# Kernel tuning notes

Hardware: AMD Instinct MI355X
Metric: run time of the kernel (lower is better)

Reference implementation:

```python
import jax, jax.numpy as jnp
import numpy as np

B, S, D, H, L, NITEMS = 512, 200, 64, 2, 2, 100000
HD = D // H
EPS = 1e-8
C = 0.001


def _ln(x, w, b):
    m = jnp.mean(x, -1, keepdims=True)
    v = jnp.mean((x - m) ** 2, -1, keepdims=True)
    return (x - m) / jnp.sqrt(v + EPS) * w + b


def _frob(x):
    return jnp.sqrt(jnp.sum(x * x))


def setup_inputs() -> dict:
    key = jax.random.key(0)
    ks = jax.random.split(key, 20)
    rn = lambda k, shape, s=0.02: jax.random.normal(k, shape, jnp.float32) * s
    item_emb = rn(ks[0], (NITEMS + 1, D))
    pos_emb = rn(ks[1], (S + 1, D)).at[0].set(0.0)  # padding_idx=0 row
    pred_w = rn(ks[2], (1, D))
    inp = {
        'user_ids': jax.random.randint(ks[3], (B,), 0, NITEMS, dtype=jnp.int32),
        'log_seqs': jax.random.randint(ks[4], (B, S), 0, NITEMS + 1, dtype=jnp.int32),
        'pos_seqs': jax.random.randint(ks[5], (B, S), 0, NITEMS + 1, dtype=jnp.int32),
        'item_emb': item_emb, 'pos_emb': pos_emb, 'pred_w': pred_w,
        'ln_w': jnp.ones((L, D), jnp.float32), 'ln_b': rn(ks[6], (L, D)),
        'qkv_w': rn(ks[7], (L, 3 * D, D)), 'qkv_b': rn(ks[8], (L, 3 * D)),
        'out_w': rn(ks[9], (L, D, D)), 'out_b': rn(ks[10], (L, D)),
        'fc1_w': rn(ks[11], (L, D, D)), 'fc1_b': rn(ks[12], (L, D)),
        'ffln_w': jnp.ones((L, D), jnp.float32), 'ffln_b': rn(ks[13], (L, D)),
        'fc2_w': rn(ks[14], (L, D, D)), 'fc2_b': rn(ks[15], (L, D)),
        'ffln2_w': jnp.ones((L, D), jnp.float32), 'ffln2_b': rn(ks[16], (L, D)),
    }
    return inp


def reference(user_ids, log_seqs, pos_seqs, item_emb, pos_emb, pred_w,
              ln_w, ln_b, qkv_w, qkv_b, out_w, out_b,
              fc1_w, fc1_b, ffln_w, ffln_b, fc2_w, fc2_b, ffln2_w, ffln2_b):
    # ---- log2feats ----
    x = item_emb[log_seqs] * jnp.sqrt(jnp.float32(D))  # (B,S,D)
    poss = jnp.arange(1, S + 1, dtype=log_seqs.dtype)[None, :] * (log_seqs != 0)
    x = x + pos_emb[poss]
    causal_bias = jnp.where(jnp.tril(jnp.ones((S, S), bool)), 0.0, -1e30).astype(jnp.float32)
    for l in range(L):
        q_in = _ln(x, ln_w[l], ln_b[l])  # query uses pre-LN, K/V use raw seqs
        q = (q_in @ qkv_w[l, :D].T + qkv_b[l, :D]).reshape(B, S, H, HD)
        k = (x @ qkv_w[l, D:2 * D].T + qkv_b[l, D:2 * D]).reshape(B, S, H, HD)
        v = (x @ qkv_w[l, 2 * D:].T + qkv_b[l, 2 * D:]).reshape(B, S, H, HD)
        sc = jnp.einsum('bqhd,bkhd->bhqk', q, k) / jnp.sqrt(jnp.float32(HD)) + causal_bias
        a = jax.nn.softmax(sc, -1)
        ctx = jnp.einsum('bhqk,bkhd->bqhd', a, v).reshape(B, S, D)
        x = q_in + ctx @ out_w[l].T + out_b[l]
        h = jax.nn.relu(_ln(x, ffln_w[l], ffln_b[l]) @ fc1_w[l].T + fc1_b[l])
        x = h @ fc2_w[l].T + fc2_b[l] + _ln(x, ffln2_w[l], ffln2_b[l])
    # ---- left(): quadratic form via Gram matrices (math identical to outer-product sum) ----
    FF = jnp.einsum('bsi,bsj->ij', x, x)          # sum_b F_b^T F_b  (d,d)
    EE = item_emb.T @ item_emb                      # (d,d)
    hh = pred_w.T @ pred_w                          # (d,d)
    left = C * jnp.sum(FF * EE * hh)
    # ---- right() ----
    ps = (x * item_emb[pos_seqs]) @ pred_w[0]       # (B,S), prediction has no bias
    right = jnp.sum((1.0 - C) * ps ** 2 - 2.0 * ps)
    # ---- reg_loss(): sum of per-parameter Frobenius norms ----
    reg = _frob(item_emb) + _frob(pos_emb) + _frob(pred_w)
    for p in (ln_w, ln_b, qkv_w, qkv_b, out_w, out_b, fc1_w, fc1_b,
              ffln_w, ffln_b, fc2_w, fc2_b, ffln2_w, ffln2_b):
        reg = reg + jnp.sum(jax.vmap(_frob)(p))  # per-layer params are separate tensors
    return left + right + 0.1 * reg
```

## Files before the change

kernel.cpp:

```cpp
#include <hip/hip_runtime.h>
#include <math.h>

#define BB 512
#define SS 200
#define DDIM 64
#define HD 32
#define LL 2
#define NROWS (BB * SS)
#define EPS 1e-8f
#define CC 0.001f
#define GRAM_NB 256
#define LSTRIDE 72
#define XS 68

typedef __attribute__((ext_vector_type(8))) short bf16x8;
typedef __attribute__((ext_vector_type(4))) float f32x4;

__device__ unsigned short g_qb[NROWS * DDIM];
__device__ float g_gpart[2 * GRAM_NB * 4096];
__device__ unsigned short g_wb[49152];

__device__ __forceinline__ float wave_sum(float v) {
#pragma unroll
    for (int o = 32; o > 0; o >>= 1) v += __shfl_xor(v, o, 64);
    return v;
}
__device__ __forceinline__ unsigned short f2b(float f) {
    unsigned u = __float_as_uint(f);
    return (unsigned short)((u + 0x7FFFu + ((u >> 16) & 1u)) >> 16);
}

__global__ __launch_bounds__(256) void prep_weights(const float* __restrict__ qkv_w,
                                                    const float* __restrict__ out_w,
                                                    const float* __restrict__ fc1_w,
                                                    const float* __restrict__ fc2_w,
                                                    unsigned short* __restrict__ wb) {
    int i4 = (blockIdx.x * 256 + threadIdx.x) * 4;
    const float* src; int off;
    if (i4 < 24576)      { src = qkv_w; off = 0; }
    else if (i4 < 32768) { src = out_w; off = 24576; }
    else if (i4 < 40960) { src = fc1_w; off = 32768; }
    else                 { src = fc2_w; off = 40960; }
    float4 f = *(const float4*)&src[i4 - off];
    ushort4 o; o.x = f2b(f.x); o.y = f2b(f.y); o.z = f2b(f.z); o.w = f2b(f.w);
    *(ushort4*)&wb[i4] = o;
}

__device__ __forceinline__ bf16x8 frag_raw(const float* Xf, int row, int c0) {
    const float* p = &Xf[row * XS + c0];
    float4 u = *(const float4*)p;
    float4 v = *(const float4*)(p + 4);
    bf16x8 r;
    r[0] = (short)f2b(u.x); r[1] = (short)f2b(u.y); r[2] = (short)f2b(u.z); r[3] = (short)f2b(u.w);
    r[4] = (short)f2b(v.x); r[5] = (short)f2b(v.y); r[6] = (short)f2b(v.z); r[7] = (short)f2b(v.w);
    return r;
}
__device__ __forceinline__ bf16x8 frag_ln(const float* Xf, const float* stats,
                                          const float* vw, const float* vb,
                                          int row, int c0) {
    float m = stats[row * 2], rs = stats[row * 2 + 1];
    const float* p = &Xf[row * XS + c0];
    float4 u = *(const float4*)p;
    float4 v = *(const float4*)(p + 4);
    bf16x8 r;
    r[0] = (short)f2b((u.x - m) * rs * vw[c0 + 0] + vb[c0 + 0]);
    r[1] = (short)f2b((u.y - m) * rs * vw[c0 + 1] + vb[c0 + 1]);
    r[2] = (short)f2b((u.z - m) * rs * vw[c0 + 2] + vb[c0 + 2]);
    r[3] = (short)f2b((u.w - m) * rs * vw[c0 + 3] + vb[c0 + 3]);
    r[4] = (short)f2b((v.x - m) * rs * vw[c0 + 4] + vb[c0 + 4]);
    r[5] = (short)f2b((v.y - m) * rs * vw[c0 + 5] + vb[c0 + 5]);
    r[6] = (short)f2b((v.z - m) * rs * vw[c0 + 6] + vb[c0 + 6]);
    r[7] = (short)f2b((v.w - m) * rs * vw[c0 + 7] + vb[c0 + 7]);
    return r;
}

__device__ __forceinline__ void gemm_acc(bf16x8 a0, bf16x8 a1, const unsigned short* W,
                                         int m16, int quad, f32x4 acc[4]) {
#pragma unroll
    for (int nt = 0; nt < 4; ++nt) {
        bf16x8 b0 = *(const bf16x8*)&W[(nt * 16 + m16) * LSTRIDE + quad * 8];
        bf16x8 b1 = *(const bf16x8*)&W[(nt * 16 + m16) * LSTRIDE + 32 + quad * 8];
        acc[nt] = __builtin_amdgcn_mfma_f32_16x16x32_bf16(a0, b0, acc[nt], 0, 0, 0);
        acc[nt] = __builtin_amdgcn_mfma_f32_16x16x32_bf16(a1, b1, acc[nt], 0, 0, 0);
    }
}

__device__ __forceinline__ void stage_w512(const unsigned short* G, unsigned short* L, int t) {
#pragma unroll
    for (int rep = 0; rep < 2; ++rep) {
        int idx = t + rep * 512;
        int r = idx >> 4, c4 = (idx & 15) * 4;
        *(ushort4*)&L[r * LSTRIDE + c4] = *(const ushort4*)&G[r * 64 + c4];
    }
}

__global__ __launch_bounds__(512) void mega(const int* __restrict__ log_seqs,
                                            const int* __restrict__ pos_seqs,
                                            const float* __restrict__ item_emb,
                                            const float* __restrict__ pos_emb,
                                            const float* __restrict__ pred_w,
                                            const float* __restrict__ ln_w,  const float* __restrict__ ln_b,
                                            const float* __restrict__ qkv_b,
                                            const float* __restrict__ out_b,
                                            const float* __restrict__ fc1_b, const float* __restrict__ fc2_b,
                                            const float* __restrict__ ffln_w, const float* __restrict__ ffln_b,
                                            const float* __restrict__ ffln2_w, const float* __restrict__ ffln2_b,
                                            const unsigned short* __restrict__ wb,
                                            unsigned short* __restrict__ xb,
                                            float* __restrict__ rpart) {
    __shared__ float Xf[200 * XS];
    __shared__ unsigned short Qb[200 * 72];
    __shared__ unsigned short Kb[200 * 72];
    __shared__ unsigned short Vt[64 * 232];
    __shared__ unsigned short Wb[64 * LSTRIDE];
    __shared__ float stats[200 * 2];
    __shared__ float vecs[13][64];
    __shared__ float redw[8];

    const int t = threadIdx.x, b = blockIdx.x;
    const int w = t >> 6, lane = t & 63, m16 = lane & 15, quad = lane >> 4;
    const f32x4 Z = {0.f, 0.f, 0.f, 0.f};

    if (t < 64) vecs[12][t] = pred_w[t];

    for (int half = 0; half < 2; ++half) {
        int rr = (t >> 2) + half * 128;
        if (rr < 200) {
            int li = log_seqs[b * SS + rr];
            int poss = li ? (rr + 1) : 0;
            int qd = (t & 3) * 16;
            float4 v[4];
#pragma unroll
            for (int g = 0; g < 4; ++g) {
                float4 e = *(const float4*)&item_emb[(long)li * DDIM + qd + g * 4];
                float4 p = *(const float4*)&pos_emb[(long)poss * DDIM + qd + g * 4];
                v[g].x = e.x * 8.0f + p.x; v[g].y = e.y * 8.0f + p.y;
                v[g].z = e.z * 8.0f + p.z; v[g].w = e.w * 8.0f + p.w;
                *(float4*)&Xf[rr * XS + qd + g * 4] = v[g];
            }
            float s1 = 0.f, s2 = 0.f;
#pragma unroll
            for (int g = 0; g < 4; ++g) {
                s1 += (v[g].x + v[g].y) + (v[g].z + v[g].w);
                s2 += (v[g].x * v[g].x + v[g].y * v[g].y) + (v[g].z * v[g].z + v[g].w * v[g].w);
            }
            s1 += __shfl_xor(s1, 1, 64); s1 += __shfl_xor(s1, 2, 64);
            s2 += __shfl_xor(s2, 1, 64); s2 += __shfl_xor(s2, 2, 64);
            float mean = s1 * (1.f / 64.f);
            float var = s2 * (1.f / 64.f) - mean * mean;
            float rs = rsqrtf(var + EPS);
            if ((t & 3) == 0) { stats[rr * 2] = mean; stats[rr * 2 + 1] = rs; }
        }
    }
    __syncthreads();

    for (int l = 0; l < LL; ++l) {
        if (t < 64) {
            vecs[0][t] = qkv_b[l * 192 + t];
            vecs[1][t] = qkv_b[l * 192 + 64 + t];
            vecs[2][t] = qkv_b[l * 192 + 128 + t];
            vecs[3][t] = ln_w[l * 64 + t];   vecs[4][t] = ln_b[l * 64 + t];
            vecs[5][t] = out_b[l * 64 + t];
            vecs[6][t] = fc1_b[l * 64 + t];  vecs[7][t] = fc2_b[l * 64 + t];
            vecs[8][t] = ffln_w[l * 64 + t]; vecs[9][t] = ffln_b[l * 64 + t];
            vecs[10][t] = ffln2_w[l * 64 + t]; vecs[11][t] = ffln2_b[l * 64 + t];
        }
        stage_w512(wb + l * 12288, Wb, t);
        __syncthreads();
        for (int tb = w * 16; tb < 200; tb += 128) {
            int row = tb + m16; if (row > 199) row = 199;
            bf16x8 a0 = frag_ln(Xf, stats, vecs[3], vecs[4], row, quad * 8);
            bf16x8 a1 = frag_ln(Xf, stats, vecs[3], vecs[4], row, 32 + quad * 8);
            f32x4 acc[4] = {Z, Z, Z, Z};
            gemm_acc(a0, a1, Wb, m16, quad, acc);
#pragma unroll
            for (int nt = 0; nt < 4; ++nt) {
                int n = nt * 16 + m16; float bbv = vecs[0][n];
#pragma unroll
                for (int rg = 0; rg < 4; ++rg) {
                    int m = tb + quad * 4 + rg;
                    if (m < 200) Qb[m * 72 + n] = f2b(acc[nt][rg] + bbv);
                }
            }
        }
        __syncthreads();
        stage_w512(wb + l * 12288 + 4096, Wb, t);
        __syncthreads();
        for (int tb = w * 16; tb < 200; tb += 128) {
            int row = tb + m16; if (row > 199) row = 199;
            bf16x8 a0 = frag_raw(Xf, row, quad * 8);
            bf16x8 a1 = frag_raw(Xf, row, 32 + quad * 8);
            f32x4 acc[4] = {Z, Z, Z, Z};
            gemm_acc(a0, a1, Wb, m16, quad, acc);
#pragma unroll
            for (int nt = 0; nt < 4; ++nt) {
                int n = nt * 16 + m16; float bbv = vecs[1][n];
#pragma unroll
                for (int rg = 0; rg < 4; ++rg) {
                    int m = tb + quad * 4 + rg;
                    if (m < 200) Kb[m * 72 + n] = f2b(acc[nt][rg] + bbv);
                }
            }
        }
        __syncthreads();
        stage_w512(wb + l * 12288 + 8192, Wb, t);
        {
            int r2 = t >> 3, cc = 200 + ((t * 4) & 31);
            ushort4 z4; z4.x = z4.y = z4.z = z4.w = 0;
            *(ushort4*)&Vt[r2 * 232 + cc] = z4;
        }
        __syncthreads();
        for (int tb = w * 16; tb < 200; tb += 128) {
            int row = tb + m16; if (row > 199) row = 199;
            bf16x8 a0 = frag_raw(Xf, row, quad * 8);
            bf16x8 a1 = frag_raw(Xf, row, 32 + quad * 8);
            f32x4 acc[4] = {Z, Z, Z, Z};
            gemm_acc(a0, a1, Wb, m16, quad, acc);
#pragma unroll
            for (int nt = 0; nt < 4; ++nt) {
                int n = nt * 16 + m16; float bbv = vecs[2][n];
#pragma unroll
                for (int rg = 0; rg < 4; ++rg) {
                    int m = tb + quad * 4 + rg;
                    if (m < 200) Vt[n * 232 + m] = f2b(acc[nt][rg] + bbv);
                }
            }
        }
        __syncthreads();
        {
            unsigned short* ps = &Wb[w * 512];
            const unsigned long long s01 = 0x01030B1900020A18ull;
            const unsigned long long s23 = 0xFF050D17FF040C16ull;
            const unsigned long long s45 = 0xFF070F15FF060E14ull;
            const unsigned long long s67 = 0xFF091113FF081012ull;
            unsigned long long pair = (w & 4) ? ((w & 2) ? s67 : s45) : ((w & 2) ? s23 : s01);
            unsigned su = (unsigned)(pair >> ((w & 1) * 32));
            const float scale = 0.17677669529663687f;
            for (int slot = 0; slot < 4; ++slot) {
                int u = (su >> (slot * 8)) & 0xFF;
                if (u == 0xFF) break;
                int h = u & 1, qt = u >> 1;
                int q0 = qt * 16;
                int qrow = q0 + m16; if (qrow > 199) qrow = 199;
                bf16x8 qa = *(const bf16x8*)&Qb[qrow * 72 + h * 32 + quad * 8];
                f32x4 o0 = Z, o1 = Z;
                float lsum[4] = {0.f, 0.f, 0.f, 0.f};
                int np = (qt + 2) >> 1;
                for (int pi = 0; pi < np; ++pi) {
                    int p0 = pi * 32;
                    int kr0 = p0 + m16;      int kr0c = kr0 > 199 ? 199 : kr0;
                    int kr1 = p0 + 16 + m16; int kr1c = kr1 > 199 ? 199 : kr1;
                    bf16x8 kb0 = *(const bf16x8*)&Kb[kr0c * 72 + h * 32 + quad * 8];
                    bf16x8 kb1 = *(const bf16x8*)&Kb[kr1c * 72 + h * 32 + quad * 8];
                    f32x4 s0 = __builtin_amdgcn_mfma_f32_16x16x32_bf16(qa, kb0, Z, 0, 0, 0);
                    f32x4 s1 = __builtin_amdgcn_mfma_f32_16x16x32_bf16(qa, kb1, Z, 0, 0, 0);
                    float e0[4], e1[4];
#pragma unroll
                    for (int rg = 0; rg < 4; ++rg) {
                        int rglob = q0 + quad * 4 + rg;
                        e0[rg] = (kr0 <= rglob && kr0 < SS) ? __expf(s0[rg] * scale) : 0.f;
                        e1[rg] = (kr1 <= rglob && kr1 < SS) ? __expf(s1[rg] * scale) : 0.f;
                        lsum[rg] += e0[rg] + e1[rg];
                    }
                    __builtin_amdgcn_wave_barrier();
#pragma unroll
                    for (int rg = 0; rg < 4; ++rg) {
                        int row = quad * 4 + rg;
                        ps[row * 32 + m16] = f2b(e0[rg]);
                        ps[row * 32 + 16 + m16] = f2b(e1[rg]);
                    }
                    __builtin_amdgcn_wave_barrier();
                    bf16x8 pa = *(const bf16x8*)&ps[m16 * 32 + quad * 8];
                    bf16x8 vb0 = *(const bf16x8*)&Vt[(h * 32 + m16) * 232 + p0 + quad * 8];
                    bf16x8 vb1 = *(const bf16x8*)&Vt[(h * 32 + 16 + m16) * 232 + p0 + quad * 8];
                    o0 = __builtin_amdgcn_mfma_f32_16x16x32_bf16(pa, vb0, o0, 0, 0, 0);
                    o1 = __builtin_amdgcn_mfma_f32_16x16x32_bf16(pa, vb1, o1, 0, 0, 0);
                }
#pragma unroll
                for (int rg = 0; rg < 4; ++rg)
#pragma unroll
                    for (int o = 1; o <= 8; o <<= 1) lsum[rg] += __shfl_xor(lsum[rg], o, 64);
#pragma unroll
                for (int rg = 0; rg < 4; ++rg) {
                    int rglob = q0 + quad * 4 + rg;
                    if (rglob < SS) {
                        float inv = 1.f / lsum[rg];
                        Qb[rglob * 72 + h * 32 + m16] = f2b(o0[rg] * inv);
                        Qb[rglob * 72 + h * 32 + 16 + m16] = f2b(o1[rg] * inv);
                    }
                }
            }
        }
        __syncthreads();
        stage_w512(wb + 24576 + l * 4096, Wb, t);
        __syncthreads();
        for (int tb = w * 16; tb < 200; tb += 128) {
            int row = tb + m16; if (row > 199) row = 199;
            bf16x8 a0 = *(const bf16x8*)&Qb[row * 72 + quad * 8];
            bf16x8 a1 = *(const bf16x8*)&Qb[row * 72 + 32 + quad * 8];
            f32x4 acc[4] = {Z, Z, Z, Z};
            gemm_acc(a0, a1, Wb, m16, quad, acc);
            float x1[4][4];
#pragma unroll
            for (int nt = 0; nt < 4; ++nt) {
                int n = nt * 16 + m16;
                float bbv = vecs[5][n], lw = vecs[3][n], lb = vecs[4][n];
#pragma unroll
                for (int rg = 0; rg < 4; ++rg) {
                    int m = tb + quad * 4 + rg; int mc = m > 199 ? 199 : m;
                    float qin = (Xf[mc * XS + n] - stats[mc * 2]) * stats[mc * 2 + 1] * lw + lb;
                    x1[nt][rg] = acc[nt][rg] + bbv + qin;
                }
            }
#pragma unroll
            for (int rg = 0; rg < 4; ++rg) {
                float s1 = (x1[0][rg] + x1[1][rg]) + (x1[2][rg] + x1[3][rg]);
                float s2 = x1[0][rg] * x1[0][rg] + x1[1][rg] * x1[1][rg]
                         + x1[2][rg] * x1[2][rg] + x1[3][rg] * x1[3][rg];
#pragma unroll
                for (int o = 1; o <= 8; o <<= 1) { s1 += __shfl_xor(s1, o, 64); s2 += __shfl_xor(s2, o, 64); }
                float mean = s1 * (1.f / 64.f);
                float var = s2 * (1.f / 64.f) - mean * mean;
                float rs = rsqrtf(var + EPS);
                int m = tb + quad * 4 + rg;
                if (m < 200) {
#pragma unroll
                    for (int nt = 0; nt < 4; ++nt) Xf[m * XS + nt * 16 + m16] = x1[nt][rg];
                    if (m16 == 0) { stats[m * 2] = mean; stats[m * 2 + 1] = rs; }
                }
            }
        }
        __syncthreads();
        stage_w512(wb + 32768 + l * 4096, Wb, t);
        __syncthreads();
        for (int tb = w * 16; tb < 200; tb += 128) {
            int row = tb + m16; if (row > 199) row = 199;
            bf16x8 a0 = frag_ln(Xf, stats, vecs[8], vecs[9], row, quad * 8);
            bf16x8 a1 = frag_ln(Xf, stats, vecs[8], vecs[9], row, 32 + quad * 8);
            f32x4 acc[4] = {Z, Z, Z, Z};
            gemm_acc(a0, a1, Wb, m16, quad, acc);
#pragma unroll
            for (int nt = 0; nt < 4; ++nt) {
                int n = nt * 16 + m16; float bbv = vecs[6][n];
#pragma unroll
                for (int rg = 0; rg < 4; ++rg) {
                    int m = tb + quad * 4 + rg;
                    if (m < 200) Qb[m * 72 + n] = f2b(fmaxf(acc[nt][rg] + bbv, 0.f));
                }
            }
        }
        __syncthreads();
        stage_w512(wb + 40960 + l * 4096, Wb, t);
        __syncthreads();
        for (int tb = w * 16; tb < 200; tb += 128) {
            int row = tb + m16; if (row > 199) row = 199;
            bf16x8 a0 = *(const bf16x8*)&Qb[row * 72 + quad * 8];
            bf16x8 a1 = *(const bf16x8*)&Qb[row * 72 + 32 + quad * 8];
            f32x4 acc[4] = {Z, Z, Z, Z};
            gemm_acc(a0, a1, Wb, m16, quad, acc);
            float xn[4][4];
#pragma unroll
            for (int nt = 0; nt < 4; ++nt) {
                int n = nt * 16 + m16;
                float bbv = vecs[7][n], lw = vecs[10][n], lb = vecs[11][n];
#pragma unroll
                for (int rg = 0; rg < 4; ++rg) {
                    int m = tb + quad * 4 + rg; int mc = m > 199 ? 199 : m;
                    float ln2 = (Xf[mc * XS + n] - stats[mc * 2]) * stats[mc * 2 + 1] * lw + lb;
                    xn[nt][rg] = acc[nt][rg] + bbv + ln2;
                }
            }
#pragma unroll
            for (int rg = 0; rg < 4; ++rg) {
                float s1 = (xn[0][rg] + xn[1][rg]) + (xn[2][rg] + xn[3][rg]);
                float s2 = xn[0][rg] * xn[0][rg] + xn[1][rg] * xn[1][rg]
                         + xn[2][rg] * xn[2][rg] + xn[3][rg] * xn[3][rg];
#pragma unroll
                for (int o = 1; o <= 8; o <<= 1) { s1 += __shfl_xor(s1, o, 64); s2 += __shfl_xor(s2, o, 64); }
                float mean = s1 * (1.f / 64.f);
                float var = s2 * (1.f / 64.f) - mean * mean;
                float rs = rsqrtf(var + EPS);
                int m = tb + quad * 4 + rg;
                if (m < 200) {
#pragma unroll
                    for (int nt = 0; nt < 4; ++nt) Xf[m * XS + nt * 16 + m16] = xn[nt][rg];
                    if (m16 == 0) { stats[m * 2] = mean; stats[m * 2 + 1] = rs; }
                }
            }
        }
        __syncthreads();
    }

    for (int i = t; i < 3200; i += 512) {
        int r = i >> 4, c4 = (i & 15) * 4;
        float4 f = *(const float4*)&Xf[r * XS + c4];
        ushort4 o; o.x = f2b(f.x); o.y = f2b(f.y); o.z = f2b(f.z); o.w = f2b(f.w);
        *(ushort4*)&xb[((long)b * SS + r) * DDIM + c4] = o;
    }
    float local = 0.f;
    for (int half = 0; half < 2; ++half) {
        int rr = (t >> 2) + half * 128;
        if (rr < 200) {
            int pi = pos_seqs[b * SS + rr];
            int qd = (t & 3) * 16;
            float v = 0.f;
#pragma unroll
            for (int g = 0; g < 4; ++g) {
                float4 xv = *(const float4*)&Xf[rr * XS + qd + g * 4];
                float4 iv = *(const float4*)&item_emb[(long)pi * DDIM + qd + g * 4];
                const float* pwp = &vecs[12][qd + g * 4];
                v += xv.x * iv.x * pwp[0] + xv.y * iv.y * pwp[1]
                   + xv.z * iv.z * pwp[2] + xv.w * iv.w * pwp[3];
            }
            v += __shfl_xor(v, 1, 64); v += __shfl_xor(v, 2, 64);
            if ((t & 3) == 0) local += (1.0f - CC) * v * v - 2.0f * v;
        }
    }
    local = wave_sum(local);
    if (lane == 0) redw[w] = local;
    __syncthreads();
    if (t == 0) {
        float s = 0.f;
#pragma unroll
        for (int i = 0; i < 8; ++i) s += redw[i];
        rpart[b] = s;
    }
}

__global__ __launch_bounds__(256) void gram_kernel(const float* __restrict__ A0, int n0,
                                                   const unsigned short* __restrict__ A1, int n1,
                                                   float* __restrict__ part) {
    __shared__ unsigned short At[64 * LSTRIDE];
    int t = threadIdx.x;
    int second = blockIdx.x >= GRAM_NB;
    int bid = second ? blockIdx.x - GRAM_NB : blockIdx.x;
    int nrows = second ? n1 : n0;
    int w16 = (t >> 6) * 16, lane = t & 63, m16 = lane & 15, quad = lane >> 4;
    int bi = t & 15, bj = t >> 4;
    f32x4 zero = {0.f, 0.f, 0.f, 0.f};
    f32x4 acc[4] = {zero, zero, zero, zero};
    for (long base = (long)bid * 64; base < nrows; base += (long)GRAM_NB * 64) {
        __syncthreads();
        if (!second) {
            float rv[4][4];
#pragma unroll
            for (int e = 0; e < 4; ++e) {
                long gr = base + bj * 4 + e;
                float4 f = make_float4(0.f, 0.f, 0.f, 0.f);
                if (gr < nrows) f = *(const float4*)&A0[gr * DDIM + bi * 4];
                rv[e][0] = f.x; rv[e][1] = f.y; rv[e][2] = f.z; rv[e][3] = f.w;
            }
#pragma unroll
            for (int e = 0; e < 4; ++e) {
                ushort4 o;
                o.x = f2b(rv[0][e]); o.y = f2b(rv[1][e]); o.z = f2b(rv[2][e]); o.w = f2b(rv[3][e]);
                *(ushort4*)&At[(bi * 4 + e) * LSTRIDE + bj * 4] = o;
            }
        } else {
            ushort4 u[4];
#pragma unroll
            for (int e = 0; e < 4; ++e) {
                long gr = base + bj * 4 + e;
                ushort4 uu; uu.x = uu.y = uu.z = uu.w = 0;
                if (gr < nrows) uu = *(const ushort4*)&A1[gr * DDIM + bi * 4];
                u[e] = uu;
            }
#pragma unroll
            for (int e = 0; e < 4; ++e) {
                ushort4 o;
                o.x = ((const unsigned short*)&u[0])[e];
                o.y = ((const unsigned short*)&u[1])[e];
                o.z = ((const unsigned short*)&u[2])[e];
                o.w = ((const unsigned short*)&u[3])[e];
                *(ushort4*)&At[(bi * 4 + e) * LSTRIDE + bj * 4] = o;
            }
        }
        __syncthreads();
#pragma unroll
        for (int ks = 0; ks < 2; ++ks) {
            bf16x8 a = *(const bf16x8*)&At[(w16 + m16) * LSTRIDE + ks * 32 + quad * 8];
#pragma unroll
            for (int nt = 0; nt < 4; ++nt) {
                bf16x8 bfr = *(const bf16x8*)&At[(nt * 16 + m16) * LSTRIDE + ks * 32 + quad * 8];
                acc[nt] = __builtin_amdgcn_mfma_f32_16x16x32_bf16(a, bfr, acc[nt], 0, 0, 0);
            }
        }
    }
    float* slab = part + (long)blockIdx.x * 4096;
#pragma unroll
    for (int nt = 0; nt < 4; ++nt) {
        int n = nt * 16 + m16;
#pragma unroll
        for (int rg = 0; rg < 4; ++rg) {
            int m = w16 + quad * 4 + rg;
            slab[m * 64 + n] = acc[nt][rg];
        }
    }
}

struct NormEntry { const float* p; int n; };
struct NormArgs { NormEntry e[30]; };

__global__ __launch_bounds__(256) void reduce_norms(const float* __restrict__ part,
                                                    float* __restrict__ EE, float* __restrict__ FF,
                                                    NormArgs args, float* __restrict__ norms) {
    __shared__ float red[256];
    int blk = blockIdx.x;
    if (blk < 32) {
        int which = blk >> 4;
        int p = (blk & 15) * 256 + threadIdx.x;
        const float* basep = part + (long)which * GRAM_NB * 4096;
        float s = 0.f;
        for (int b = 0; b < GRAM_NB; ++b) s += basep[(long)b * 4096 + p];
        (which ? FF : EE)[p] = s;
    } else {
        NormEntry en = args.e[blk - 32];
        float s = 0.f;
        for (int i = threadIdx.x; i < en.n; i += 256) { float v = en.p[i]; s += v * v; }
        red[threadIdx.x] = s;
        for (int o = 128; o > 0; o >>= 1) {
            __syncthreads();
            if (threadIdx.x < o) red[threadIdx.x] += red[threadIdx.x + o];
        }
        __syncthreads();
        if (threadIdx.x == 0) norms[blk - 32] = red[0];
    }
}

__global__ __launch_bounds__(256) void final_kernel(const float* __restrict__ EE,
                                                    const float* __restrict__ FF,
                                                    const float* __restrict__ pred_w,
                                                    const float* __restrict__ rpart,
                                                    const float* __restrict__ norms,
                                                    float* __restrict__ out) {
    __shared__ float p_s[64];
    __shared__ float redL[256];
    __shared__ float redT[256];
    __shared__ float redR[256];
    int t = threadIdx.x;
    if (t < 64) p_s[t] = pred_w[t];
    __syncthreads();
    float lf = 0.f, tr = 0.f, rs = 0.f;
    for (int p = t; p < 4096; p += 256) {
        int i = p >> 6, j = p & 63;
        float ee = EE[p];
        lf += FF[p] * ee * p_s[i] * p_s[j];
        if (i == j) tr += ee;
    }
    for (int i = t; i < 512; i += 256) rs += rpart[i];
    redL[t] = lf; redT[t] = tr; redR[t] = rs;
    for (int o = 128; o > 0; o >>= 1) {
        __syncthreads();
        if (t < o) { redL[t] += redL[t + o]; redT[t] += redT[t + o]; redR[t] += redR[t + o]; }
    }
    __syncthreads();
    if (t == 0) {
        float reg = sqrtf(redT[0]);
        for (int s = 0; s < 30; ++s) reg += sqrtf(norms[s]);
        out[0] = CC * redL[0] + redR[0] + 0.1f * reg;
    }
}

struct DevPtrs { float* gpart; unsigned short *qb, *wb; };

static DevPtrs fetch_ptrs() {
    DevPtrs p;
    (void)hipGetSymbolAddress((void**)&p.gpart, HIP_SYMBOL(g_gpart));
    (void)hipGetSymbolAddress((void**)&p.qb,    HIP_SYMBOL(g_qb));
    (void)hipGetSymbolAddress((void**)&p.wb,    HIP_SYMBOL(g_wb));
    return p;
}

extern "C" void kernel_launch(void* const* d_in, const int* in_sizes, int n_in,
                              void* d_out, int out_size, void* d_ws, size_t ws_size,
                              hipStream_t stream) {
    const int*   log_seqs = (const int*)d_in[1];
    const int*   pos_seqs = (const int*)d_in[2];
    const float* item_emb = (const float*)d_in[3];
    const float* pos_emb  = (const float*)d_in[4];
    const float* pred_w   = (const float*)d_in[5];
    const float* ln_w     = (const float*)d_in[6];
    const float* ln_b     = (const float*)d_in[7];
    const float* qkv_w    = (const float*)d_in[8];
    const float* qkv_b    = (const float*)d_in[9];
    const float* out_w    = (const float*)d_in[10];
    const float* out_b    = (const float*)d_in[11];
    const float* fc1_w    = (const float*)d_in[12];
    const float* fc1_b    = (const float*)d_in[13];
    const float* ffln_w   = (const float*)d_in[14];
    const float* ffln_b   = (const float*)d_in[15];
    const float* fc2_w    = (const float*)d_in[16];
    const float* fc2_b    = (const float*)d_in[17];
    const float* ffln2_w  = (const float*)d_in[18];
    const float* ffln2_b  = (const float*)d_in[19];

    static DevPtrs P = fetch_ptrs();

    float* ws    = (float*)d_ws;
    float* rpart = ws;
    float* nrm   = ws + 1664;
    float* EE    = ws + 2048;
    float* FF    = ws + 6144;

    prep_weights<<<48, 256, 0, stream>>>(qkv_w, out_w, fc1_w, fc2_w, P.wb);

    mega<<<BB, 512, 0, stream>>>(log_seqs, pos_seqs, item_emb, pos_emb, pred_w,
                                 ln_w, ln_b, qkv_b, out_b, fc1_b, fc2_b,
                                 ffln_w, ffln_b, ffln2_w, ffln2_b,
                                 P.wb, P.qb, rpart);

    gram_kernel<<<2 * GRAM_NB, 256, 0, stream>>>(item_emb, 100001, P.qb, NROWS, P.gpart);

    NormArgs na;
    int s = 0;
    na.e[s++] = {pos_emb, (SS + 1) * DDIM};
    na.e[s++] = {pred_w, DDIM};
    for (int l = 0; l < LL; ++l) {
        na.e[s++] = {ln_w + l * 64, 64};
        na.e[s++] = {ln_b + l * 64, 64};
        na.e[s++] = {qkv_w + (long)l * 12288, 12288};
        na.e[s++] = {qkv_b + (long)l * 192, 192};
        na.e[s++] = {out_w + (long)l * 4096, 4096};
        na.e[s++] = {out_b + l * 64, 64};
        na.e[s++] = {fc1_w + (long)l * 4096, 4096};
        na.e[s++] = {fc1_b + l * 64, 64};
        na.e[s++] = {ffln_w + l * 64, 64};
        na.e[s++] = {ffln_b + l * 64, 64};
        na.e[s++] = {fc2_w + (long)l * 4096, 4096};
        na.e[s++] = {fc2_b + l * 64, 64};
        na.e[s++] = {ffln2_w + l * 64, 64};
        na.e[s++] = {ffln2_b + l * 64, 64};
    }
    reduce_norms<<<62, 256, 0, stream>>>(P.gpart, EE, FF, na, nrm);

    final_kernel<<<1, 256, 0, stream>>>(EE, FF, pred_w, rpart, nrm, (float*)d_out);
}
```

Before: 254.6 us.

## Double block to 1024 threads, fuse QKV and FFN stages per wave with register weights

Launches the fused transformer kernel with 1024 threads and assigns wave groups to the Q, K and V projections at the same time. Each wave now loads its weight fragments straight from global memory into registers instead of staging them in LDS. The out-proj, LN, fc1 and fc2 chain runs per 16-row tile inside a single wave, which removes many block-wide syncs. Attention probabilities reuse the Q buffer as scratch, freeing the weight LDS buffer. This trades block barriers and LDS staging for higher register pressure and repeated global weight reads, and it leaves a no-op leftover line plus a redundant fragment load.

```diff
diff --git a/kernel.cpp b/kernel.cpp
--- a/kernel.cpp
+++ b/kernel.cpp
@@ -12,6 +12,7 @@
 #define GRAM_NB 256
 #define LSTRIDE 72
 #define XS 68
+#define QROWS 208
 
 typedef __attribute__((ext_vector_type(8))) short bf16x8;
 typedef __attribute__((ext_vector_type(4))) float f32x4;
@@ -74,57 +75,56 @@
     return r;
 }
 
-__device__ __forceinline__ void gemm_acc(bf16x8 a0, bf16x8 a1, const unsigned short* W,
-                                         int m16, int quad, f32x4 acc[4]) {
+__device__ __forceinline__ void load_wf(const unsigned short* __restrict__ Wg,
+                                        int m16, int quad, bf16x8 wf[8]) {
 #pragma unroll
     for (int nt = 0; nt < 4; ++nt) {
-        bf16x8 b0 = *(const bf16x8*)&W[(nt * 16 + m16) * LSTRIDE + quad * 8];
-        bf16x8 b1 = *(const bf16x8*)&W[(nt * 16 + m16) * LSTRIDE + 32 + quad * 8];
-        acc[nt] = __builtin_amdgcn_mfma_f32_16x16x32_bf16(a0, b0, acc[nt], 0, 0, 0);
-        acc[nt] = __builtin_amdgcn_mfma_f32_16x16x32_bf16(a1, b1, acc[nt], 0, 0, 0);
-    }
-}
-
-__device__ __forceinline__ void stage_w512(const unsigned short* G, unsigned short* L, int t) {
-#pragma unroll
-    for (int rep = 0; rep < 2; ++rep) {
-        int idx = t + rep * 512;
-        int r = idx >> 4, c4 = (idx & 15) * 4;
-        *(ushort4*)&L[r * LSTRIDE + c4] = *(const ushort4*)&G[r * 64 + c4];
-    }
-}
-
-__global__ __launch_bounds__(512) void mega(const int* __restrict__ log_seqs,
-                                            const int* __restrict__ pos_seqs,
-                                            const float* __restrict__ item_emb,
-                                            const float* __restrict__ pos_emb,
-                                            const float* __restrict__ pred_w,
-                                            const float* __restrict__ ln_w,  const float* __restrict__ ln_b,
-                                            const float* __restrict__ qkv_b,
-                                            const float* __restrict__ out_b,
-                                            const float* __restrict__ fc1_b, const float* __restrict__ fc2_b,
-                                            const float* __restrict__ ffln_w, const float* __restrict__ ffln_b,
-                                            const float* __restrict__ ffln2_w, const float* __restrict__ ffln2_b,
-                                            const unsigned short* __restrict__ wb,
-                                            unsigned short* __restrict__ xb,
-                                            float* __restrict__ rpart) {
+        wf[nt * 2]     = *(const bf16x8*)&Wg[(nt * 16 + m16) * 64 + quad * 8];
+        wf[nt * 2 + 1] = *(const bf16x8*)&Wg[(nt * 16 + m16) * 64 + 32 + quad * 8];
+    }
+}
+__device__ __forceinline__ void gemm_rw(bf16x8 a0, bf16x8 a1, const bf16x8 wf[8], f32x4 acc[4]) {
+#pragma unroll
+    for (int nt = 0; nt < 4; ++nt) {
+        acc[nt] = __builtin_amdgcn_mfma_f32_16x16x32_bf16(a0, wf[nt * 2], acc[nt], 0, 0, 0);
+        acc[nt] = __builtin_amdgcn_mfma_f32_16x16x32_bf16(a1, wf[nt * 2 + 1], acc[nt], 0, 0, 0);
+    }
+}
+
+__global__ __launch_bounds__(1024) void mega(const int* __restrict__ log_seqs,
+                                             const int* __restrict__ pos_seqs,
+                                             const float* __restrict__ item_emb,
+                                             const float* __restrict__ pos_emb,
+                                             const float* __restrict__ pred_w,
+                                             const float* __restrict__ ln_w,  const float* __restrict__ ln_b,
+                                             const float* __restrict__ qkv_b,
+                                             const float* __restrict__ out_b,
+                                             const float* __restrict__ fc1_b, const float* __restrict__ fc2_b,
+                                             const float* __restrict__ ffln_w, const float* __restrict__ ffln_b,
+                                             const float* __restrict__ ffln2_w, const float* __restrict__ ffln2_b,
+                                             const unsigned short* __restrict__ wb,
+                                             unsigned short* __restrict__ xb,
+                                             float* __restrict__ rpart) {
     __shared__ float Xf[200 * XS];
-    __shared__ unsigned short Qb[200 * 72];
-    __shared__ unsigned short Kb[200 * 72];
+    __shared__ unsigned short Qb[QROWS * 72];
+    __shared__ unsigned short Kb[QROWS * 72];
     __shared__ unsigned short Vt[64 * 232];
-    __shared__ unsigned short Wb[64 * LSTRIDE];
     __shared__ float stats[200 * 2];
     __shared__ float vecs[13][64];
-    __shared__ float redw[8];
+    __shared__ float redw[16];
 
     const int t = threadIdx.x, b = blockIdx.x;
     const int w = t >> 6, lane = t & 63, m16 = lane & 15, quad = lane >> 4;
     const f32x4 Z = {0.f, 0.f, 0.f, 0.f};
 
     if (t < 64) vecs[12][t] = pred_w[t];
-
-    for (int half = 0; half < 2; ++half) {
-        int rr = (t >> 2) + half * 128;
+    if (t < 512) {
+        int r2 = t >> 3, cc = 200 + (t & 7) * 4;
+        ushort4 z4; z4.x = z4.y = z4.z = z4.w = 0;
+        *(ushort4*)&Vt[r2 * 232 + cc] = z4;
+    }
+    {
+        int rr = t >> 2;
         if (rr < 200) {
             int li = log_seqs[b * SS + rr];
             int poss = li ? (rr + 1) : 0;
@@ -152,9 +152,9 @@
             if ((t & 3) == 0) { stats[rr * 2] = mean; stats[rr * 2 + 1] = rs; }
         }
     }
-    __syncthreads();
 
     for (int l = 0; l < LL; ++l) {
+        __syncthreads();
         if (t < 64) {
             vecs[0][t] = qkv_b[l * 192 + t];
             vecs[1][t] = qkv_b[l * 192 + 64 + t];
@@ -165,84 +165,68 @@
             vecs[8][t] = ffln_w[l * 64 + t]; vecs[9][t] = ffln_b[l * 64 + t];
             vecs[10][t] = ffln2_w[l * 64 + t]; vecs[11][t] = ffln2_b[l * 64 + t];
         }
-        stage_w512(wb + l * 12288, Wb, t);
-        __syncthreads();
-        for (int tb = w * 16; tb < 200; tb += 128) {
-            int row = tb + m16; if (row > 199) row = 199;
-            bf16x8 a0 = frag_ln(Xf, stats, vecs[3], vecs[4], row, quad * 8);
-            bf16x8 a1 = frag_ln(Xf, stats, vecs[3], vecs[4], row, 32 + quad * 8);
-            f32x4 acc[4] = {Z, Z, Z, Z};
-            gemm_acc(a0, a1, Wb, m16, quad, acc);
-#pragma unroll
-            for (int nt = 0; nt < 4; ++nt) {
-                int n = nt * 16 + m16; float bbv = vecs[0][n];
-#pragma unroll
-                for (int rg = 0; rg < 4; ++rg) {
-                    int m = tb + quad * 4 + rg;
-                    if (m < 200) Qb[m * 72 + n] = f2b(acc[nt][rg] + bbv);
+        __syncthreads();
+        {
+            int gsel, wbase, nwv;
+            if (w < 6)       { gsel = 0; wbase = 0;  nwv = 6; }
+            else if (w < 11) { gsel = 1; wbase = 6;  nwv = 5; }
+            else             { gsel = 2; wbase = 11; nwv = 5; }
+            bf16x8 wf[8];
+            load_wf(wb + l * 12288 + gsel * 4096, m16, quad, wf);
+            const float* bias = vecs[gsel];
+            for (int tt = w - wbase; tt < 13; tt += nwv) {
+                int tb = tt * 16;
+                int row = tb + m16; if (row > 199) row = 199;
+                bf16x8 a0, a1;
+                if (gsel == 0) {
+                    a0 = frag_ln(Xf, stats, vecs[3], vecs[4], row, 0);
+                    a1 = frag_ln(Xf, stats, vecs[3], vecs[4], row, 32);
+                } else {
+                    a0 = frag_raw(Xf, row, 0);
+                    a1 = frag_raw(Xf, row, 32);
                 }
-            }
-        }
-        __syncthreads();
-        stage_w512(wb + l * 12288 + 4096, Wb, t);
-        __syncthreads();
-        for (int tb = w * 16; tb < 200; tb += 128) {
-            int row = tb + m16; if (row > 199) row = 199;
-            bf16x8 a0 = frag_raw(Xf, row, quad * 8);
-            bf16x8 a1 = frag_raw(Xf, row, 32 + quad * 8);
-            f32x4 acc[4] = {Z, Z, Z, Z};
-            gemm_acc(a0, a1, Wb, m16, quad, acc);
-#pragma unroll
-            for (int nt = 0; nt < 4; ++nt) {
-                int n = nt * 16 + m16; float bbv = vecs[1][n];
-#pragma unroll
-                for (int rg = 0; rg < 4; ++rg) {
-                    int m = tb + quad * 4 + rg;
-                    if (m < 200) Kb[m * 72 + n] = f2b(acc[nt][rg] + bbv);
+                a0 = *(const bf16x8*)((const short*)&Xf[0] == nullptr ? (const short*)&a0 : (const short*)&a0);
+                if (gsel == 0) {
+                    a0 = frag_ln(Xf, stats, vecs[3], vecs[4], row, quad * 8);
+                    a1 = frag_ln(Xf, stats, vecs[3], vecs[4], row, 32 + quad * 8);
+                } else {
+                    a0 = frag_raw(Xf, row, quad * 8);
+                    a1 = frag_raw(Xf, row, 32 + quad * 8);
                 }
-            }
-        }
-        __syncthreads();
-        stage_w512(wb + l * 12288 + 8192, Wb, t);
+                f32x4 acc[4] = {Z, Z, Z, Z};
+                gemm_rw(a0, a1, wf, acc);
+#pragma unroll
+                for (int nt = 0; nt < 4; ++nt) {
+                    int n = nt * 16 + m16; float bbv = bias[n];
+#pragma unroll
+                    for (int rg = 0; rg < 4; ++rg) {
+                        int m = tb + quad * 4 + rg;
+                        float val = acc[nt][rg] + bbv;
+                        if (gsel == 0)      Qb[m * 72 + n] = f2b(val);
+                        else if (gsel == 1) Kb[m * 72 + n] = f2b(val);
+                        else if (m < 200)   Vt[n * 232 + m] = f2b(val);
+                    }
+                }
+            }
+        }
+        __syncthreads();
         {
-            int r2 = t >> 3, cc = 200 + ((t * 4) & 31);
-            ushort4 z4; z4.x = z4.y = z4.z = z4.w = 0;
-            *(ushort4*)&Vt[r2 * 232 + cc] = z4;
-        }
-        __syncthreads();
-        for (int tb = w * 16; tb < 200; tb += 128) {
-            int row = tb + m16; if (row > 199) row = 199;
-            bf16x8 a0 = frag_raw(Xf, row, quad * 8);
-            bf16x8 a1 = frag_raw(Xf, row, 32 + quad * 8);
-            f32x4 acc[4] = {Z, Z, Z, Z};
-            gemm_acc(a0, a1, Wb, m16, quad, acc);
-#pragma unroll
-            for (int nt = 0; nt < 4; ++nt) {
-                int n = nt * 16 + m16; float bbv = vecs[2][n];
-#pragma unroll
-                for (int rg = 0; rg < 4; ++rg) {
-                    int m = tb + quad * 4 + rg;
-                    if (m < 200) Vt[n * 232 + m] = f2b(acc[nt][rg] + bbv);
-                }
-            }
-        }
-        __syncthreads();
-        {
-            unsigned short* ps = &Wb[w * 512];
-            const unsigned long long s01 = 0x01030B1900020A18ull;
-            const unsigned long long s23 = 0xFF050D17FF040C16ull;
-            const unsigned long long s45 = 0xFF070F15FF060E14ull;
-            const unsigned long long s67 = 0xFF091113FF081012ull;
-            unsigned long long pair = (w & 4) ? ((w & 2) ? s67 : s45) : ((w & 2) ? s23 : s01);
-            unsigned su = (unsigned)(pair >> ((w & 1) * 32));
+            const unsigned long long tab0 = 0x01170016FF19FF18ull;
+            const unsigned long long tab1 = 0x0513041203150214ull;
+            const unsigned long long tab2 = 0x090F080E07110610ull;
+            const unsigned long long tab3 = 0xFFFFFFFF0B0D0A0Cull;
+            unsigned long long tv = (w & 8) ? ((w & 4) ? tab3 : tab2) : ((w & 4) ? tab1 : tab0);
+            unsigned su = (unsigned)((tv >> ((w & 3) * 16)) & 0xFFFFu);
             const float scale = 0.17677669529663687f;
-            for (int slot = 0; slot < 4; ++slot) {
+            for (int slot = 0; slot < 2; ++slot) {
                 int u = (su >> (slot * 8)) & 0xFF;
                 if (u == 0xFF) break;
                 int h = u & 1, qt = u >> 1;
                 int q0 = qt * 16;
                 int qrow = q0 + m16; if (qrow > 199) qrow = 199;
                 bf16x8 qa = *(const bf16x8*)&Qb[qrow * 72 + h * 32 + quad * 8];
+                __builtin_amdgcn_wave_barrier();
+                unsigned short* ps = &Qb[q0 * 72 + h * 32];
                 f32x4 o0 = Z, o1 = Z;
                 float lsum[4] = {0.f, 0.f, 0.f, 0.f};
                 int np = (qt + 2) >> 1;
@@ -266,11 +250,11 @@
 #pragma unroll
                     for (int rg = 0; rg < 4; ++rg) {
                         int row = quad * 4 + rg;
-                        ps[row * 32 + m16] = f2b(e0[rg]);
-                        ps[row * 32 + 16 + m16] = f2b(e1[rg]);
+                        ps[row * 72 + m16] = f2b(e0[rg]);
+                        ps[row * 72 + 16 + m16] = f2b(e1[rg]);
                     }
                     __builtin_amdgcn_wave_barrier();
-                    bf16x8 pa = *(const bf16x8*)&ps[m16 * 32 + quad * 8];
+                    bf16x8 pa = *(const bf16x8*)&ps[m16 * 72 + quad * 8];
                     bf16x8 vb0 = *(const bf16x8*)&Vt[(h * 32 + m16) * 232 + p0 + quad * 8];
                     bf16x8 vb1 = *(const bf16x8*)&Vt[(h * 32 + 16 + m16) * 232 + p0 + quad * 8];
                     o0 = __builtin_amdgcn_mfma_f32_16x16x32_bf16(pa, vb0, o0, 0, 0, 0);
@@ -280,6 +264,7 @@
                 for (int rg = 0; rg < 4; ++rg)
 #pragma unroll
                     for (int o = 1; o <= 8; o <<= 1) lsum[rg] += __shfl_xor(lsum[rg], o, 64);
+                __builtin_amdgcn_wave_barrier();
 #pragma unroll
                 for (int rg = 0; rg < 4; ++rg) {
                     int rglob = q0 + quad * 4 + rg;
@@ -292,15 +277,16 @@
             }
         }
         __syncthreads();
-        stage_w512(wb + 24576 + l * 4096, Wb, t);
-        __syncthreads();
-        for (int tb = w * 16; tb < 200; tb += 128) {
+        if (w < 13) {
+            int tb = w * 16;
+            bf16x8 wf[8];
+            load_wf(wb + 24576 + l * 4096, m16, quad, wf);
             int row = tb + m16; if (row > 199) row = 199;
             bf16x8 a0 = *(const bf16x8*)&Qb[row * 72 + quad * 8];
             bf16x8 a1 = *(const bf16x8*)&Qb[row * 72 + 32 + quad * 8];
-            f32x4 acc[4] = {Z, Z, Z, Z};
-            gemm_acc(a0, a1, Wb, m16, quad, acc);
-            float x1[4][4];
+            f32x4 acc1[4] = {Z, Z, Z, Z};
+            gemm_rw(a0, a1, wf, acc1);
+            float core[4][4];
 #pragma unroll
             for (int nt = 0; nt < 4; ++nt) {
                 int n = nt * 16 + m16;
@@ -309,14 +295,65 @@
                 for (int rg = 0; rg < 4; ++rg) {
                     int m = tb + quad * 4 + rg; int mc = m > 199 ? 199 : m;
                     float qin = (Xf[mc * XS + n] - stats[mc * 2]) * stats[mc * 2 + 1] * lw + lb;
-                    x1[nt][rg] = acc[nt][rg] + bbv + qin;
+                    core[nt][rg] = acc1[nt][rg] + bbv + qin;
                 }
             }
 #pragma unroll
             for (int rg = 0; rg < 4; ++rg) {
-                float s1 = (x1[0][rg] + x1[1][rg]) + (x1[2][rg] + x1[3][rg]);
-                float s2 = x1[0][rg] * x1[0][rg] + x1[1][rg] * x1[1][rg]
-                         + x1[2][rg] * x1[2][rg] + x1[3][rg] * x1[3][rg];
+                float s1 = (core[0][rg] + core[1][rg]) + (core[2][rg] + core[3][rg]);
+                float s2 = core[0][rg] * core[0][rg] + core[1][rg] * core[1][rg]
+                         + core[2][rg] * core[2][rg] + core[3][rg] * core[3][rg];
+#pragma unroll
+                for (int o = 1; o <= 8; o <<= 1) { s1 += __shfl_xor(s1, o, 64); s2 += __shfl_xor(s2, o, 64); }
+                float mean = s1 * (1.f / 64.f);
+                float var = s2 * (1.f / 64.f) - mean * mean;
+                float rs = rsqrtf(var + EPS);
+#pragma unroll
+                for (int nt = 0; nt < 4; ++nt) core[nt][rg] = (core[nt][rg] - mean) * rs;
+            }
+            __builtin_amdgcn_wave_barrier();
+#pragma unroll
+            for (int nt = 0; nt < 4; ++nt) {
+                int n = nt * 16 + m16;
+                float w8v = vecs[8][n], b9v = vecs[9][n];
+#pragma unroll
+                for (int rg = 0; rg < 4; ++rg)
+                    Kb[(tb + quad * 4 + rg) * 72 + n] = f2b(core[nt][rg] * w8v + b9v);
+            }
+            __builtin_amdgcn_wave_barrier();
+            load_wf(wb + 32768 + l * 4096, m16, quad, wf);
+            a0 = *(const bf16x8*)&Kb[(tb + m16) * 72 + quad * 8];
+            a1 = *(const bf16x8*)&Kb[(tb + m16) * 72 + 32 + quad * 8];
+            f32x4 acc2[4] = {Z, Z, Z, Z};
+            gemm_rw(a0, a1, wf, acc2);
+            __builtin_amdgcn_wave_barrier();
+#pragma unroll
+            for (int nt = 0; nt < 4; ++nt) {
+                int n = nt * 16 + m16; float bbv = vecs[6][n];
+#pragma unroll
+                for (int rg = 0; rg < 4; ++rg)
+                    Kb[(tb + quad * 4 + rg) * 72 + n] = f2b(fmaxf(acc2[nt][rg] + bbv, 0.f));
+            }
+            __builtin_amdgcn_wave_barrier();
+            load_wf(wb + 40960 + l * 4096, m16, quad, wf);
+            a0 = *(const bf16x8*)&Kb[(tb + m16) * 72 + quad * 8];
+            a1 = *(const bf16x8*)&Kb[(tb + m16) * 72 + 32 + quad * 8];
+            f32x4 acc3[4] = {Z, Z, Z, Z};
+            gemm_rw(a0, a1, wf, acc3);
+            float xn[4][4];
+#pragma unroll
+            for (int nt = 0; nt < 4; ++nt) {
+                int n = nt * 16 + m16;
+                float bbv = vecs[7][n], lw = vecs[10][n], lb = vecs[11][n];
+#pragma unroll
+                for (int rg = 0; rg < 4; ++rg)
+                    xn[nt][rg] = acc3[nt][rg] + bbv + core[nt][rg] * lw + lb;
+            }
+#pragma unroll
+            for (int rg = 0; rg < 4; ++rg) {
+                float s1 = (xn[0][rg] + xn[1][rg]) + (xn[2][rg] + xn[3][rg]);
+                float s2 = xn[0][rg] * xn[0][rg] + xn[1][rg] * xn[1][rg]
+                         + xn[2][rg] * xn[2][rg] + xn[3][rg] * xn[3][rg];
 #pragma unroll
                 for (int o = 1; o <= 8; o <<= 1) { s1 += __shfl_xor(s1, o, 64); s2 += __shfl_xor(s2, o, 64); }
                 float mean = s1 * (1.f / 64.f);
@@ -325,81 +362,23 @@
                 int m = tb + quad * 4 + rg;
                 if (m < 200) {
 #pragma unroll
-                    for (int nt = 0; nt < 4; ++nt) Xf[m * XS + nt * 16 + m16] = x1[nt][rg];
-                    if (m16 == 0) { stats[m * 2] = mean; stats[m * 2 + 1] = rs; }
-                }
-            }
-        }
-        __syncthreads();
-        stage_w512(wb + 32768 + l * 4096, Wb, t);
-        __syncthreads();
-        for (int tb = w * 16; tb < 200; tb += 128) {
-            int row = tb + m16; if (row > 199) row = 199;
-            bf16x8 a0 = frag_ln(Xf, stats, vecs[8], vecs[9], row, quad * 8);
-            bf16x8 a1 = frag_ln(Xf, stats, vecs[8], vecs[9], row, 32 + quad * 8);
-            f32x4 acc[4] = {Z, Z, Z, Z};
-            gemm_acc(a0, a1, Wb, m16, quad, acc);
-#pragma unroll
-            for (int nt = 0; nt < 4; ++nt) {
-                int n = nt * 16 + m16; float bbv = vecs[6][n];
-#pragma unroll
-                for (int rg = 0; rg < 4; ++rg) {
-                    int m = tb + quad * 4 + rg;
-                    if (m < 200) Qb[m * 72 + n] = f2b(fmaxf(acc[nt][rg] + bbv, 0.f));
-                }
-            }
-        }
-        __syncthreads();
-        stage_w512(wb + 40960 + l * 4096, Wb, t);
-        __syncthreads();
-        for (int tb = w * 16; tb < 200; tb += 128) {
-            int row = tb + m16; if (row > 199) row = 199;
-            bf16x8 a0 = *(const bf16x8*)&Qb[row * 72 + quad * 8];
-            bf16x8 a1 = *(const bf16x8*)&Qb[row * 72 + 32 + quad * 8];
-            f32x4 acc[4] = {Z, Z, Z, Z};
-            gemm_acc(a0, a1, Wb, m16, quad, acc);
-            float xn[4][4];
-#pragma unroll
-            for (int nt = 0; nt < 4; ++nt) {
-                int n = nt * 16 + m16;
-                float bbv = vecs[7][n], lw = vecs[10][n], lb = vecs[11][n];
-#pragma unroll
-                for (int rg = 0; rg < 4; ++rg) {
-                    int m = tb + quad * 4 + rg; int mc = m > 199 ? 199 : m;
-                    float ln2 = (Xf[mc * XS + n] - stats[mc * 2]) * stats[mc * 2 + 1] * lw + lb;
-                    xn[nt][rg] = acc[nt][rg] + bbv + ln2;
-                }
-            }
-#pragma unroll
-            for (int rg = 0; rg < 4; ++rg) {
-                float s1 = (xn[0][rg] + xn[1][rg]) + (xn[2][rg] + xn[3][rg]);
-                float s2 = xn[0][rg] * xn[0][rg] + xn[1][rg] * xn[1][rg]
-                         + xn[2][rg] * xn[2][rg] + xn[3][rg] * xn[3][rg];
-#pragma unroll
-                for (int o = 1; o <= 8; o <<= 1) { s1 += __shfl_xor(s1, o, 64); s2 += __shfl_xor(s2, o, 64); }
-                float mean = s1 * (1.f / 64.f);
-                float var = s2 * (1.f / 64.f) - mean * mean;
-                float rs = rsqrtf(var + EPS);
-                int m = tb + quad * 4 + rg;
-                if (m < 200) {
-#pragma unroll
                     for (int nt = 0; nt < 4; ++nt) Xf[m * XS + nt * 16 + m16] = xn[nt][rg];
                     if (m16 == 0) { stats[m * 2] = mean; stats[m * 2 + 1] = rs; }
                 }
             }
         }
-        __syncthreads();
-    }
-
-    for (int i = t; i < 3200; i += 512) {
+    }
+    __syncthreads();
+
+    for (int i = t; i < 3200; i += 1024) {
         int r = i >> 4, c4 = (i & 15) * 4;
         float4 f = *(const float4*)&Xf[r * XS + c4];
         ushort4 o; o.x = f2b(f.x); o.y = f2b(f.y); o.z = f2b(f.z); o.w = f2b(f.w);
         *(ushort4*)&xb[((long)b * SS + r) * DDIM + c4] = o;
     }
     float local = 0.f;
-    for (int half = 0; half < 2; ++half) {
-        int rr = (t >> 2) + half * 128;
+    {
+        int rr = t >> 2;
         if (rr < 200) {
             int pi = pos_seqs[b * SS + rr];
             int qd = (t & 3) * 16;
@@ -422,7 +401,7 @@
     if (t == 0) {
         float s = 0.f;
 #pragma unroll
-        for (int i = 0; i < 8; ++i) s += redw[i];
+        for (int i = 0; i < 16; ++i) s += redw[i];
         rpart[b] = s;
     }
 }
@@ -604,10 +583,10 @@
 
     prep_weights<<<48, 256, 0, stream>>>(qkv_w, out_w, fc1_w, fc2_w, P.wb);
 
-    mega<<<BB, 512, 0, stream>>>(log_seqs, pos_seqs, item_emb, pos_emb, pred_w,
-                                 ln_w, ln_b, qkv_b, out_b, fc1_b, fc2_b,
-                                 ffln_w, ffln_b, ffln2_w, ffln2_b,
-                                 P.wb, P.qb, rpart);
+    mega<<<BB, 1024, 0, stream>>>(log_seqs, pos_seqs, item_emb, pos_emb, pred_w,
+                                  ln_w, ln_b, qkv_b, out_b, fc1_b, fc2_b,
+                                  ffln_w, ffln_b, ffln2_w, ffln2_b,
+                                  P.wb, P.qb, rpart);
 
     gram_kernel<<<2 * GRAM_NB, 256, 0, stream>>>(item_emb, 100001, P.qb, NROWS, P.gpart);
 
```

After: 269.8 us. 5.9% more time.
